# Performance work log

Measured on AMD Instinct MI355X. Metric: run time of the kernel, lower is better.

Reference implementation:

```python
import jax, jax.numpy as jnp
import numpy as np

D = 256      # embed_dims
NH = 8       # num_heads
NL = 1       # num_levels
NP = 6       # num_points
BS = 1
NQ = 40000   # 200x200 BEV queries
H0, W0 = 200, 200
HD = D // NH


def _ln(x, g, b):
    m = jnp.mean(x, -1, keepdims=True)
    v = jnp.var(x, -1, keepdims=True)
    return (x - m) / jnp.sqrt(v + 1e-5) * g + b


def _bilinear(v, lx, ly, H, W):
    # v: (bs, h, H*W, hd); lx/ly: (bs, h, S) pixel coords (align_corners=False, zero padding)
    x0 = jnp.floor(lx).astype(jnp.int32)
    y0 = jnp.floor(ly).astype(jnp.int32)
    acc = 0.
    for dx in (0, 1):
        for dy in (0, 1):
            xi = x0 + dx
            yi = y0 + dy
            w = (1. - jnp.abs(lx - xi)) * (1. - jnp.abs(ly - yi))
            valid = (xi >= 0) & (xi < W) & (yi >= 0) & (yi < H)
            idx = jnp.clip(yi, 0, H - 1) * W + jnp.clip(xi, 0, W - 1)
            g = jnp.take_along_axis(v, idx[..., None], axis=2)  # (bs,h,S,hd)
            acc = acc + g * (w * valid)[..., None]
    return acc


def _forward(query, value, reference_points, W_off, b_off, W_attn, b_attn,
             W_val, b_val, W_out, b_out, ln1_g, ln1_b, W1, b1, W2, b2,
             ln2_g, ln2_b, ss, lsi):
    bs, nq, d = query.shape
    # sampling offsets and attention weights from the query
    off = (query @ W_off + b_off).reshape(bs, nq, NH, NL, NP, 2)
    attn = jax.nn.softmax((query @ W_attn + b_attn).reshape(bs, nq, NH, NL * NP), -1)
    attn = attn.reshape(bs, nq, NH, NL, NP)
    v = (value @ W_val + b_val).reshape(bs, -1, NH, HD).transpose(0, 2, 1, 3)  # (bs,h,HW,hd)
    # offset normalizer is [W, H] per level
    norm = jnp.stack([ss[:, 1], ss[:, 0]], -1).astype(query.dtype)  # (NL,2)
    loc = reference_points[:, :, None, :, None, :] + off / norm[None, None, None, :, None, :]
    out = jnp.zeros((bs, NH, nq, HD), query.dtype)
    for l in range(NL):
        Hl = int(ss[l, 0]); Wl = int(ss[l, 1]); st = int(lsi[l])
        vl = v[:, :, st:st + Hl * Wl]
        lx = (loc[:, :, :, l, :, 0] * Wl - 0.5).transpose(0, 2, 1, 3).reshape(bs, NH, nq * NP)
        ly = (loc[:, :, :, l, :, 1] * Hl - 0.5).transpose(0, 2, 1, 3).reshape(bs, NH, nq * NP)
        sampled = _bilinear(vl, lx, ly, Hl, Wl).reshape(bs, NH, nq, NP, HD)
        wl = attn[:, :, :, l, :].transpose(0, 2, 1, 3)  # (bs,h,nq,P)
        out = out + jnp.einsum('bhqp,bhqpd->bhqd', wl, sampled)
    y_msda = out.transpose(0, 2, 1, 3).reshape(bs, nq, d) @ W_out + b_out
    y = _ln(y_msda + query, ln1_g, ln1_b)
    y_ffn = jax.nn.gelu(y @ W1 + b1, approximate=False) @ W2 + b2
    return _ln(y_ffn + y, ln2_g, ln2_b)


def setup_inputs():
    key = jax.random.key(0)
    ks = jax.random.split(key, 12)
    s = 0.02
    return {
        'query': jax.random.normal(ks[0], (BS, NQ, D), jnp.float32),
        'value': jax.random.normal(ks[1], (BS, H0 * W0, D), jnp.float32),
        'reference_points': jax.random.uniform(ks[2], (BS, NQ, NL, 2), jnp.float32),
        'spatial_shapes': jnp.array([[H0, W0]], jnp.int32),
        'level_start_index': jnp.array([0], jnp.int32),
        'W_off': jax.random.normal(ks[3], (D, NH * NL * NP * 2), jnp.float32) * s,
        'b_off': jax.random.uniform(ks[4], (NH * NL * NP * 2,), jnp.float32, -1., 1.),
        'W_attn': jax.random.normal(ks[5], (D, NH * NL * NP), jnp.float32) * s,
        'b_attn': jnp.zeros((NH * NL * NP,), jnp.float32),
        'W_val': jax.random.normal(ks[6], (D, D), jnp.float32) * s,
        'b_val': jnp.zeros((D,), jnp.float32),
        'W_out': jax.random.normal(ks[7], (D, D), jnp.float32) * s,
        'b_out': jnp.zeros((D,), jnp.float32),
        'ln1_g': jnp.ones((D,), jnp.float32),
        'ln1_b': jnp.zeros((D,), jnp.float32),
        'W1': jax.random.normal(ks[8], (D, D), jnp.float32) * s,
        'b1': jnp.zeros((D,), jnp.float32),
        'W2': jax.random.normal(ks[9], (D, D), jnp.float32) * s,
        'b2': jnp.zeros((D,), jnp.float32),
        'ln2_g': jnp.ones((D,), jnp.float32),
        'ln2_b': jnp.zeros((D,), jnp.float32),
    }


def reference(query, value, reference_points, spatial_shapes, level_start_index,
              W_off, b_off, W_attn, b_attn, W_val, b_val, W_out, b_out,
              ln1_g, ln1_b, W1, b1, W2, b2, ln2_g, ln2_b):
    ss = np.asarray(spatial_shapes)
    lsi = np.asarray(level_start_index)
    return _forward(query, value, reference_points, W_off, b_off, W_attn, b_attn,
                    W_val, b_val, W_out, b_out, ln1_g, ln1_b, W1, b1, W2, b2,
                    ln2_g, ln2_b, ss, lsi)
```

## Files before the change

kernel.cpp:

```cpp
#include <hip/hip_runtime.h>
#include <math.h>

#define NQ 40000
#define DIM 256
#define NH 8
#define NP 6
#define HD 32
#define GH 200
#define GW 200
#define TS 8
#define TNX 25
#define NT 625

typedef short bf16x8 __attribute__((ext_vector_type(8)));
typedef float f32x4 __attribute__((ext_vector_type(4)));

__device__ __forceinline__ unsigned short f2bf(float f) {
    unsigned int u = __builtin_bit_cast(unsigned int, f);
    u += 0x7fffu + ((u >> 16) & 1u);
    return (unsigned short)(u >> 16);
}
__device__ __forceinline__ float bf2f(unsigned short h) {
    return __builtin_bit_cast(float, ((unsigned int)h) << 16);
}

__global__ void __launch_bounds__(256)
f2b_kernel(const float* __restrict__ q, unsigned short* __restrict__ qd,
           const float* __restrict__ v, unsigned short* __restrict__ vd) {
    int b = blockIdx.x;
    const float* src; unsigned short* dst;
    if (b < 5000) { src = q; dst = qd; } else { src = v; dst = vd; b -= 5000; }
    const int i = b * 256 + threadIdx.x;
    const float4* s = (const float4*)src;
    float4 a = s[(size_t)i * 2], c = s[(size_t)i * 2 + 1];
    bf16x8 o;
    o[0] = (short)f2bf(a.x); o[1] = (short)f2bf(a.y);
    o[2] = (short)f2bf(a.z); o[3] = (short)f2bf(a.w);
    o[4] = (short)f2bf(c.x); o[5] = (short)f2bf(c.y);
    o[6] = (short)f2bf(c.z); o[7] = (short)f2bf(c.w);
    *(bf16x8*)(dst + (size_t)i * 8) = o;
}

__global__ void __launch_bounds__(256)
wtrans_kernel(const float* __restrict__ Wval, const float* __restrict__ Woff,
              const float* __restrict__ Wattn, const float* __restrict__ Wout,
              const float* __restrict__ W1, const float* __restrict__ W2,
              const float* __restrict__ b_off, const float* __restrict__ b_attn,
              unsigned short* __restrict__ Bt, float* __restrict__ bias_oa) {
    __shared__ float T[64][65];
    const int m = blockIdx.z;
    const float* src; int N; int dr0;
    if (m == 0)      { src = Wval;  N = 256; dr0 = 0; }
    else if (m == 1) { src = Woff;  N = 96;  dr0 = 256; }
    else if (m == 2) { src = Wattn; N = 48;  dr0 = 352; }
    else if (m == 3) { src = Wout;  N = 256; dr0 = 400; }
    else if (m == 4) { src = W1;    N = 256; dr0 = 656; }
    else             { src = W2;    N = 256; dr0 = 912; }

    if (m == 1 && blockIdx.x == 0 && blockIdx.y == 0 && threadIdx.x < 144)
        bias_oa[threadIdx.x] = threadIdx.x < 96 ? b_off[threadIdx.x]
                                                : b_attn[threadIdx.x - 96];

    const int n0 = blockIdx.x * 64, k0 = blockIdx.y * 64;
    if (n0 >= N) return;
    const int col = threadIdx.x & 63, rg = threadIdx.x >> 6;
#pragma unroll
    for (int i = 0; i < 16; ++i) {
        const int r = rg + 4 * i;
        T[r][col] = (n0 + col < N) ? src[(size_t)(k0 + r) * N + n0 + col] : 0.0f;
    }
    __syncthreads();
#pragma unroll
    for (int i = 0; i < 16; ++i) {
        const int nl = rg + 4 * i;
        if (n0 + nl < N)
            Bt[(size_t)(dr0 + n0 + nl) * 256 + k0 + col] = f2bf(T[col][nl]);
    }
}

__device__ __forceinline__ int tile_of(const float* rp, int q) {
    const float rx = rp[q * 2 + 0] * (float)GW;
    const float ry = rp[q * 2 + 1] * (float)GH;
    const int tx = min(max((int)(rx * (1.0f / TS)), 0), TNX - 1);
    const int ty = min(max((int)(ry * (1.0f / TS)), 0), TNX - 1);
    return ty * TNX + tx;
}

__global__ void __launch_bounds__(256)
sort_zero(int* __restrict__ hist) {
    const int i = blockIdx.x * 256 + threadIdx.x;
    if (i < NT) hist[i] = 0;
}

__global__ void __launch_bounds__(256)
sort_hist(const float* __restrict__ rp, int* __restrict__ hist) {
    const int q = blockIdx.x * 256 + threadIdx.x;
    if (q >= NQ) return;
    atomicAdd(&hist[tile_of(rp, q)], 1);
}

__global__ void __launch_bounds__(64)
sort_scan(const int* __restrict__ hist, int* __restrict__ cursor) {
    const int lane = threadIdx.x;
    int loc[10]; int t = 0;
#pragma unroll
    for (int j = 0; j < 10; ++j) {
        const int idx = lane * 10 + j;
        loc[j] = t;
        t += (idx < NT) ? hist[idx] : 0;
    }
    int s = t;
#pragma unroll
    for (int o = 1; o < 64; o <<= 1) {
        const int u = __shfl_up(s, o);
        if (lane >= o) s += u;
    }
    const int ex = s - t;
#pragma unroll
    for (int j = 0; j < 10; ++j) {
        const int idx = lane * 10 + j;
        if (idx < NT) cursor[idx] = ex + loc[j];
    }
}

__global__ void __launch_bounds__(256)
sort_scatter(const float* __restrict__ rp, int* __restrict__ cursor,
             int* __restrict__ perm) {
    const int q = blockIdx.x * 256 + threadIdx.x;
    if (q >= NQ) return;
    const int pos = atomicAdd(&cursor[tile_of(rp, q)], 1);
    perm[pos] = q;
}

template <int EPI>
__global__ void __launch_bounds__(256)
gemm_bt(const unsigned short* __restrict__ A, const unsigned short* __restrict__ Bt,
        const float* __restrict__ bias, void* __restrict__ C,
        int M, int N, int ldc) {
    __shared__ __align__(16) unsigned short As[128 * 32];
    __shared__ __align__(16) unsigned short Bs[128 * 32];

    const int tid = threadIdx.x, lane = tid & 63, wave = tid >> 6;
    const int quad = lane >> 4, l16 = lane & 15;
    const int wm = wave >> 1, wn = wave & 1;
    const int bm0 = blockIdx.y * 128, bn0 = blockIdx.x * 128;

    f32x4 acc[4][4] = {};

    const int rl = lane >> 2;
    const int c8 = (lane & 3) * 8;

    for (int kt = 0; kt < 8; ++kt) {
        const int k0 = kt * 32;
        __syncthreads();
#pragma unroll
        for (int i = 0; i < 2; ++i) {
            const int rgrp = i * 64 + wave * 16;
            const int gA = min(bm0 + rgrp + rl, M - 1);
            const unsigned short* gpa = A + (size_t)gA * 256 + k0 + c8;
            __builtin_amdgcn_global_load_lds(
                (const __attribute__((address_space(1))) void*)gpa,
                (__attribute__((address_space(3))) void*)(As + (size_t)rgrp * 32),
                16, 0, 0);
            const int gB = min(bn0 + rgrp + rl, N - 1);
            const unsigned short* gpb = Bt + (size_t)gB * 256 + k0 + c8;
            __builtin_amdgcn_global_load_lds(
                (const __attribute__((address_space(1))) void*)gpb,
                (__attribute__((address_space(3))) void*)(Bs + (size_t)rgrp * 32),
                16, 0, 0);
        }
        __syncthreads();

        bf16x8 af[4], bw[4];
#pragma unroll
        for (int t = 0; t < 4; ++t) {
            af[t] = *(const bf16x8*)&As[(wm * 64 + t * 16 + l16) * 32 + quad * 8];
            bw[t] = *(const bf16x8*)&Bs[(wn * 64 + t * 16 + l16) * 32 + quad * 8];
        }
#pragma unroll
        for (int tm = 0; tm < 4; ++tm)
#pragma unroll
            for (int tn = 0; tn < 4; ++tn)
                acc[tm][tn] = __builtin_amdgcn_mfma_f32_16x16x32_bf16(
                    af[tm], bw[tn], acc[tm][tn], 0, 0, 0);
    }

#pragma unroll
    for (int tm = 0; tm < 4; ++tm) {
        const int row0 = bm0 + wm * 64 + tm * 16 + quad * 4;
#pragma unroll
        for (int tn = 0; tn < 4; ++tn) {
            const int col = bn0 + wn * 64 + tn * 16 + l16;
            if (col < N) {
                const float bv = bias[col];
#pragma unroll
                for (int r = 0; r < 4; ++r) {
                    const int row = row0 + r;
                    if (row < M) {
                        float x = acc[tm][tn][r] + bv;
                        if (EPI == 1) {
                            x = 0.5f * x * (1.0f + erff(x * 0.70710678118654752f));
                            ((unsigned short*)C)[(size_t)row * ldc + col] = f2bf(x);
                        } else if (EPI == 2) {
                            ((unsigned short*)C)[(size_t)row * ldc + col] = f2bf(x);
                        } else {
                            ((float*)C)[(size_t)row * ldc + col] = x;
                        }
                    }
                }
            }
        }
    }
}

__global__ void __launch_bounds__(256)
msda_sample(const unsigned short* __restrict__ v,
            const unsigned short* __restrict__ oa,
            const float* __restrict__ rp,
            const int* __restrict__ perm,
            unsigned short* __restrict__ out) {
    const int b = blockIdx.x;
    const int w = (b & 7) * 625 + (b >> 3);
    const int tid = threadIdx.x;
    const int slot = tid >> 2;
    const int q = perm[w * 8 + (slot >> 3)];
    const int h = slot & 7;
    const int c0 = (tid & 3) * 8;

    const float rx = rp[q * 2 + 0] * (float)GW;
    const float ry = rp[q * 2 + 1] * (float)GH;

    const unsigned short* oaq = oa + (size_t)q * 144;
    float lg[NP];
    float mx = -1e30f;
#pragma unroll
    for (int p = 0; p < NP; ++p) {
        lg[p] = bf2f(oaq[96 + h * NP + p]);
        mx = fmaxf(mx, lg[p]);
    }
    float s = 0.0f;
#pragma unroll
    for (int p = 0; p < NP; ++p) { lg[p] = expf(lg[p] - mx); s += lg[p]; }
    const float inv = 1.0f / s;

    float acc[8] = {};
#pragma unroll
    for (int p = 0; p < NP; ++p) {
        const float aw = lg[p] * inv;
        const float lx = rx + bf2f(oaq[h * 12 + p * 2 + 0]) - 0.5f;
        const float ly = ry + bf2f(oaq[h * 12 + p * 2 + 1]) - 0.5f;
        const float fx0 = floorf(lx), fy0 = floorf(ly);
        const int x0 = (int)fx0, y0 = (int)fy0;
        const float fx = lx - fx0, fy = ly - fy0;
#pragma unroll
        for (int dy = 0; dy < 2; ++dy) {
            const int yi = y0 + dy;
            const float wyv = dy ? fy : 1.0f - fy;
#pragma unroll
            for (int dx = 0; dx < 2; ++dx) {
                const int xi = x0 + dx;
                const float wxv = dx ? fx : 1.0f - fx;
                const bool valid = (xi >= 0) & (xi < GW) & (yi >= 0) & (yi < GH);
                const int yc = min(max(yi, 0), GH - 1);
                const int xc = min(max(xi, 0), GW - 1);
                const float wgt = valid ? aw * wxv * wyv : 0.0f;
                const bf16x8 g = *(const bf16x8*)&v[((size_t)(yc * GW + xc)) * 256 + h * 32 + c0];
#pragma unroll
                for (int j = 0; j < 8; ++j)
                    acc[j] += bf2f((unsigned short)g[j]) * wgt;
            }
        }
    }
    bf16x8 o;
#pragma unroll
    for (int j = 0; j < 8; ++j) o[j] = (short)f2bf(acc[j]);
    *(bf16x8*)&out[(size_t)q * 256 + h * 32 + c0] = o;
}

template <int RES_BF, int OUT_BF>
__global__ void __launch_bounds__(256)
ln_res(const float* __restrict__ x, const void* __restrict__ res,
       const float* __restrict__ g, const float* __restrict__ b,
       void* __restrict__ out, int M) {
    const int wave = threadIdx.x >> 6;
    const int lane = threadIdx.x & 63;
    const int row = blockIdx.x * 4 + wave;
    if (row >= M) return;

    const size_t base = (size_t)row * DIM + lane * 4;
    const float4 xv = *(const float4*)(x + base);
    float e[4];
    if (RES_BF) {
        const unsigned short* rb = (const unsigned short*)res + base;
        uint2 rv = *(const uint2*)rb;
        const unsigned short* rs = (const unsigned short*)&rv;
        e[0] = xv.x + bf2f(rs[0]); e[1] = xv.y + bf2f(rs[1]);
        e[2] = xv.z + bf2f(rs[2]); e[3] = xv.w + bf2f(rs[3]);
    } else {
        const float4 rv = *(const float4*)((const float*)res + base);
        e[0] = xv.x + rv.x; e[1] = xv.y + rv.y;
        e[2] = xv.z + rv.z; e[3] = xv.w + rv.w;
    }

    float s = e[0] + e[1] + e[2] + e[3];
    float sq = e[0] * e[0] + e[1] * e[1] + e[2] * e[2] + e[3] * e[3];
#pragma unroll
    for (int o = 1; o < 64; o <<= 1) {
        s += __shfl_xor(s, o);
        sq += __shfl_xor(sq, o);
    }
    const float mean = s * (1.0f / DIM);
    const float var = sq * (1.0f / DIM) - mean * mean;
    const float rstd = rsqrtf(var + 1e-5f);

    const float4 gv = *(const float4*)(g + lane * 4);
    const float4 bv = *(const float4*)(b + lane * 4);
    float o0 = (e[0] - mean) * rstd * gv.x + bv.x;
    float o1 = (e[1] - mean) * rstd * gv.y + bv.y;
    float o2 = (e[2] - mean) * rstd * gv.z + bv.z;
    float o3 = (e[3] - mean) * rstd * gv.w + bv.w;
    if (OUT_BF) {
        unsigned short ob[4] = {f2bf(o0), f2bf(o1), f2bf(o2), f2bf(o3)};
        *(uint2*)((unsigned short*)out + base) = *(uint2*)ob;
    } else {
        float4 o4 = {o0, o1, o2, o3};
        *(float4*)((float*)out + base) = o4;
    }
}

extern "C" void kernel_launch(void* const* d_in, const int* in_sizes, int n_in,
                              void* d_out, int out_size, void* d_ws, size_t ws_size,
                              hipStream_t stream) {
    const float* query  = (const float*)d_in[0];
    const float* value  = (const float*)d_in[1];
    const float* rp     = (const float*)d_in[2];
    const float* W_off  = (const float*)d_in[5];
    const float* b_off  = (const float*)d_in[6];
    const float* W_attn = (const float*)d_in[7];
    const float* b_attn = (const float*)d_in[8];
    const float* W_val  = (const float*)d_in[9];
    const float* b_val  = (const float*)d_in[10];
    const float* W_out  = (const float*)d_in[11];
    const float* b_out  = (const float*)d_in[12];
    const float* ln1_g  = (const float*)d_in[13];
    const float* ln1_b  = (const float*)d_in[14];
    const float* W1     = (const float*)d_in[15];
    const float* b1     = (const float*)d_in[16];
    const float* W2     = (const float*)d_in[17];
    const float* b2     = (const float*)d_in[18];
    const float* ln2_g  = (const float*)d_in[19];
    const float* ln2_b  = (const float*)d_in[20];

    char* ws = (char*)d_ws;
    unsigned short* Bt       = (unsigned short*)ws;
    float*          bias_oa  = (float*)(ws + 598016);
    int*            hist     = (int*)(ws + 598592);
    int*            cursor   = (int*)(ws + 601600);
    int*            perm     = (int*)(ws + 604608);
    unsigned short* query_bf = (unsigned short*)(ws + 770048);
    unsigned short* h1_bf    = query_bf;
    unsigned short* value_bf = (unsigned short*)(ws + 21250048);
    unsigned short* msda_bf  = value_bf;
    unsigned short* y_bf     = value_bf;
    unsigned short* v_bf     = (unsigned short*)(ws + 41730048);
    unsigned short* oa_bf    = (unsigned short*)(ws + 62210048);
    float*          outp     = (float*)d_out;

    dim3 blk(256);
    f2b_kernel<<<dim3(10000), blk, 0, stream>>>(query, query_bf, value, value_bf);
    wtrans_kernel<<<dim3(4, 4, 6), blk, 0, stream>>>(W_val, W_off, W_attn, W_out, W1, W2,
                                                     b_off, b_attn, Bt, bias_oa);
    sort_zero<<<dim3(3), blk, 0, stream>>>(hist);
    sort_hist<<<dim3(157), blk, 0, stream>>>(rp, hist);
    sort_scan<<<dim3(1), dim3(64), 0, stream>>>(hist, cursor);
    sort_scatter<<<dim3(157), blk, 0, stream>>>(rp, cursor, perm);
    gemm_bt<2><<<dim3(2, 313), blk, 0, stream>>>(value_bf, Bt, b_val, (void*)v_bf, NQ, 256, 256);
    gemm_bt<2><<<dim3(2, 313), blk, 0, stream>>>(query_bf, Bt + 256 * 256, bias_oa,
                                                 (void*)oa_bf, NQ, 144, 144);
    msda_sample<<<dim3(5000), blk, 0, stream>>>(v_bf, oa_bf, rp, perm, msda_bf);
    gemm_bt<0><<<dim3(2, 313), blk, 0, stream>>>(msda_bf, Bt + 400 * 256, b_out,
                                                 (void*)outp, NQ, 256, 256);
    ln_res<0, 1><<<dim3(10000), blk, 0, stream>>>(outp, query, ln1_g, ln1_b, (void*)y_bf, NQ);
    gemm_bt<1><<<dim3(2, 313), blk, 0, stream>>>(y_bf, Bt + 656 * 256, b1,
                                                 (void*)h1_bf, NQ, 256, 256);
    gemm_bt<0><<<dim3(2, 313), blk, 0, stream>>>(h1_bf, Bt + 912 * 256, b2,
                                                 (void*)outp, NQ, 256, 256);
    ln_res<1, 0><<<dim3(10000), blk, 0, stream>>>(outp, y_bf, ln2_g, ln2_b, (void*)outp, NQ);
}
```

Measured before the change: 357.4 us.

## Fuse residual-add and LayerNorm into full-width double-buffered GEMM epilogues

Adds a 64-row by 256-column GEMM kernel with double-buffered LDS staging, so each block owns whole output rows. The output projection and second FFN GEMM now do bias, residual add and LayerNorm in the epilogue via a cross-wave LDS reduction, which removes the two separate ln_res passes and their fp32 intermediate round trips. The value projection and first FFN GEMM also move to this kernel. The cost is larger LDS use and lower occupancy per block, and the new kernel has no M bounds checks because it relies on 40000 being divisible by 64.

```diff
diff --git a/kernel.cpp b/kernel.cpp
--- a/kernel.cpp
+++ b/kernel.cpp
@@ -134,8 +134,160 @@
 
 template <int EPI>
 __global__ void __launch_bounds__(256)
+gemm64(const unsigned short* __restrict__ A, const unsigned short* __restrict__ Bt,
+       const float* __restrict__ bias, const void* __restrict__ res,
+       const float* __restrict__ lng, const float* __restrict__ lnb,
+       void* __restrict__ C, int M) {
+    __shared__ __align__(16) unsigned short As[2][64 * 32];
+    __shared__ __align__(16) unsigned short Bs[2][256 * 32];
+    __shared__ __align__(16) float red[64][4][2];
+
+    const int tid = threadIdx.x, lane = tid & 63, wave = tid >> 6;
+    const int quad = lane >> 4, l16 = lane & 15;
+    const int bm0 = blockIdx.x * 64;
+    const int r16 = lane >> 2;
+    const int ch = (lane & 3) * 8;
+
+    f32x4 acc[4][4] = {};
+
+    auto stage = [&](int kt, int buf) {
+        const int k0 = kt * 32;
+        {
+            const int row = wave * 16 + r16;
+            const unsigned short* gp = A + (size_t)(bm0 + row) * 256 + k0 + ch;
+            __builtin_amdgcn_global_load_lds(
+                (const __attribute__((address_space(1))) void*)gp,
+                (__attribute__((address_space(3))) void*)(&As[buf][wave * 16 * 32]),
+                16, 0, 0);
+        }
+#pragma unroll
+        for (int j = 0; j < 4; ++j) {
+            const int rowbase = (wave * 4 + j) * 16;
+            const unsigned short* gp = Bt + (size_t)(rowbase + r16) * 256 + k0 + ch;
+            __builtin_amdgcn_global_load_lds(
+                (const __attribute__((address_space(1))) void*)gp,
+                (__attribute__((address_space(3))) void*)(&Bs[buf][rowbase * 32]),
+                16, 0, 0);
+        }
+    };
+
+    stage(0, 0);
+    __syncthreads();
+
+    for (int kt = 0; kt < 8; ++kt) {
+        const int cur = kt & 1;
+        if (kt < 7) stage(kt + 1, 1 - cur);
+
+        bf16x8 af[4], bw[4];
+#pragma unroll
+        for (int t = 0; t < 4; ++t) {
+            af[t] = *(const bf16x8*)&As[cur][(t * 16 + l16) * 32 + quad * 8];
+            bw[t] = *(const bf16x8*)&Bs[cur][(wave * 64 + t * 16 + l16) * 32 + quad * 8];
+        }
+#pragma unroll
+        for (int tm = 0; tm < 4; ++tm)
+#pragma unroll
+            for (int tn = 0; tn < 4; ++tn)
+                acc[tm][tn] = __builtin_amdgcn_mfma_f32_16x16x32_bf16(
+                    af[tm], bw[tn], acc[tm][tn], 0, 0, 0);
+        __syncthreads();
+    }
+
+    float bias4[4];
+#pragma unroll
+    for (int tn = 0; tn < 4; ++tn) bias4[tn] = bias[wave * 64 + tn * 16 + l16];
+
+    if (EPI == 1 || EPI == 2) {
+#pragma unroll
+        for (int tm = 0; tm < 4; ++tm) {
+            const int row0 = bm0 + tm * 16 + quad * 4;
+#pragma unroll
+            for (int tn = 0; tn < 4; ++tn) {
+                const int col = wave * 64 + tn * 16 + l16;
+#pragma unroll
+                for (int r = 0; r < 4; ++r) {
+                    float x = acc[tm][tn][r] + bias4[tn];
+                    if (EPI == 1) x = 0.5f * x * (1.0f + erff(x * 0.70710678118654752f));
+                    ((unsigned short*)C)[(size_t)(row0 + r) * 256 + col] = f2bf(x);
+                }
+            }
+        }
+        return;
+    }
+
+#pragma unroll
+    for (int tm = 0; tm < 4; ++tm) {
+#pragma unroll
+        for (int r = 0; r < 4; ++r) {
+            const size_t rb = (size_t)(bm0 + tm * 16 + quad * 4 + r) * 256;
+#pragma unroll
+            for (int tn = 0; tn < 4; ++tn) {
+                const int col = wave * 64 + tn * 16 + l16;
+                float e = acc[tm][tn][r] + bias4[tn];
+                if (EPI == 3) e += ((const float*)res)[rb + col];
+                else          e += bf2f(((const unsigned short*)res)[rb + col]);
+                acc[tm][tn][r] = e;
+            }
+        }
+    }
+#pragma unroll
+    for (int tm = 0; tm < 4; ++tm) {
+#pragma unroll
+        for (int r = 0; r < 4; ++r) {
+            float s = 0.0f, sq = 0.0f;
+#pragma unroll
+            for (int tn = 0; tn < 4; ++tn) {
+                const float e = acc[tm][tn][r];
+                s += e; sq += e * e;
+            }
+#pragma unroll
+            for (int o = 1; o < 16; o <<= 1) {
+                s += __shfl_xor(s, o);
+                sq += __shfl_xor(sq, o);
+            }
+            if (l16 == 0) {
+                const int row = tm * 16 + quad * 4 + r;
+                red[row][wave][0] = s;
+                red[row][wave][1] = sq;
+            }
+        }
+    }
+    __syncthreads();
+
+    float gv[4], bvv[4];
+#pragma unroll
+    for (int tn = 0; tn < 4; ++tn) {
+        const int col = wave * 64 + tn * 16 + l16;
+        gv[tn] = lng[col];
+        bvv[tn] = lnb[col];
+    }
+#pragma unroll
+    for (int tm = 0; tm < 4; ++tm) {
+#pragma unroll
+        for (int r = 0; r < 4; ++r) {
+            const int row = tm * 16 + quad * 4 + r;
+            const float4 p0 = *(const float4*)&red[row][0][0];
+            const float4 p1 = *(const float4*)&red[row][2][0];
+            const float sum = p0.x + p0.z + p1.x + p1.z;
+            const float sumsq = p0.y + p0.w + p1.y + p1.w;
+            const float mean = sum * (1.0f / 256.0f);
+            const float var = sumsq * (1.0f / 256.0f) - mean * mean;
+            const float rstd = rsqrtf(var + 1e-5f);
+            const size_t rb = (size_t)(bm0 + row) * 256;
+#pragma unroll
+            for (int tn = 0; tn < 4; ++tn) {
+                const int col = wave * 64 + tn * 16 + l16;
+                const float o = (acc[tm][tn][r] - mean) * rstd * gv[tn] + bvv[tn];
+                if (EPI == 3) ((unsigned short*)C)[rb + col] = f2bf(o);
+                else          ((float*)C)[rb + col] = o;
+            }
+        }
+    }
+}
+
+__global__ void __launch_bounds__(256)
 gemm_bt(const unsigned short* __restrict__ A, const unsigned short* __restrict__ Bt,
-        const float* __restrict__ bias, void* __restrict__ C,
+        const float* __restrict__ bias, unsigned short* __restrict__ C,
         int M, int N, int ldc) {
     __shared__ __align__(16) unsigned short As[128 * 32];
     __shared__ __align__(16) unsigned short Bs[128 * 32];
@@ -146,7 +298,6 @@
     const int bm0 = blockIdx.y * 128, bn0 = blockIdx.x * 128;
 
     f32x4 acc[4][4] = {};
-
     const int rl = lane >> 2;
     const int c8 = (lane & 3) * 8;
 
@@ -196,17 +347,8 @@
 #pragma unroll
                 for (int r = 0; r < 4; ++r) {
                     const int row = row0 + r;
-                    if (row < M) {
-                        float x = acc[tm][tn][r] + bv;
-                        if (EPI == 1) {
-                            x = 0.5f * x * (1.0f + erff(x * 0.70710678118654752f));
-                            ((unsigned short*)C)[(size_t)row * ldc + col] = f2bf(x);
-                        } else if (EPI == 2) {
-                            ((unsigned short*)C)[(size_t)row * ldc + col] = f2bf(x);
-                        } else {
-                            ((float*)C)[(size_t)row * ldc + col] = x;
-                        }
-                    }
+                    if (row < M)
+                        C[(size_t)row * ldc + col] = f2bf(acc[tm][tn][r] + bv);
                 }
             }
         }
@@ -275,57 +417,6 @@
 #pragma unroll
     for (int j = 0; j < 8; ++j) o[j] = (short)f2bf(acc[j]);
     *(bf16x8*)&out[(size_t)q * 256 + h * 32 + c0] = o;
-}
-
-template <int RES_BF, int OUT_BF>
-__global__ void __launch_bounds__(256)
-ln_res(const float* __restrict__ x, const void* __restrict__ res,
-       const float* __restrict__ g, const float* __restrict__ b,
-       void* __restrict__ out, int M) {
-    const int wave = threadIdx.x >> 6;
-    const int lane = threadIdx.x & 63;
-    const int row = blockIdx.x * 4 + wave;
-    if (row >= M) return;
-
-    const size_t base = (size_t)row * DIM + lane * 4;
-    const float4 xv = *(const float4*)(x + base);
-    float e[4];
-    if (RES_BF) {
-        const unsigned short* rb = (const unsigned short*)res + base;
-        uint2 rv = *(const uint2*)rb;
-        const unsigned short* rs = (const unsigned short*)&rv;
-        e[0] = xv.x + bf2f(rs[0]); e[1] = xv.y + bf2f(rs[1]);
-        e[2] = xv.z + bf2f(rs[2]); e[3] = xv.w + bf2f(rs[3]);
-    } else {
-        const float4 rv = *(const float4*)((const float*)res + base);
-        e[0] = xv.x + rv.x; e[1] = xv.y + rv.y;
-        e[2] = xv.z + rv.z; e[3] = xv.w + rv.w;
-    }
-
-    float s = e[0] + e[1] + e[2] + e[3];
-    float sq = e[0] * e[0] + e[1] * e[1] + e[2] * e[2] + e[3] * e[3];
-#pragma unroll
-    for (int o = 1; o < 64; o <<= 1) {
-        s += __shfl_xor(s, o);
-        sq += __shfl_xor(sq, o);
-    }
-    const float mean = s * (1.0f / DIM);
-    const float var = sq * (1.0f / DIM) - mean * mean;
-    const float rstd = rsqrtf(var + 1e-5f);
-
-    const float4 gv = *(const float4*)(g + lane * 4);
-    const float4 bv = *(const float4*)(b + lane * 4);
-    float o0 = (e[0] - mean) * rstd * gv.x + bv.x;
-    float o1 = (e[1] - mean) * rstd * gv.y + bv.y;
-    float o2 = (e[2] - mean) * rstd * gv.z + bv.z;
-    float o3 = (e[3] - mean) * rstd * gv.w + bv.w;
-    if (OUT_BF) {
-        unsigned short ob[4] = {f2bf(o0), f2bf(o1), f2bf(o2), f2bf(o3)};
-        *(uint2*)((unsigned short*)out + base) = *(uint2*)ob;
-    } else {
-        float4 o4 = {o0, o1, o2, o3};
-        *(float4*)((float*)out + base) = o4;
-    }
 }
 
 extern "C" void kernel_launch(void* const* d_in, const int* in_sizes, int n_in,
@@ -361,8 +452,8 @@
     unsigned short* h1_bf    = query_bf;
     unsigned short* value_bf = (unsigned short*)(ws + 21250048);
     unsigned short* msda_bf  = value_bf;
-    unsigned short* y_bf     = value_bf;
     unsigned short* v_bf     = (unsigned short*)(ws + 41730048);
+    unsigned short* y_bf     = v_bf;
     unsigned short* oa_bf    = (unsigned short*)(ws + 62210048);
     float*          outp     = (float*)d_out;
 
@@ -374,16 +465,17 @@
     sort_hist<<<dim3(157), blk, 0, stream>>>(rp, hist);
     sort_scan<<<dim3(1), dim3(64), 0, stream>>>(hist, cursor);
     sort_scatter<<<dim3(157), blk, 0, stream>>>(rp, cursor, perm);
-    gemm_bt<2><<<dim3(2, 313), blk, 0, stream>>>(value_bf, Bt, b_val, (void*)v_bf, NQ, 256, 256);
-    gemm_bt<2><<<dim3(2, 313), blk, 0, stream>>>(query_bf, Bt + 256 * 256, bias_oa,
-                                                 (void*)oa_bf, NQ, 144, 144);
+    gemm64<2><<<dim3(625), blk, 0, stream>>>(value_bf, Bt, b_val, nullptr, nullptr, nullptr,
+                                             (void*)v_bf, NQ);
+    gemm_bt<<<dim3(2, 313), blk, 0, stream>>>(query_bf, Bt + 256 * 256, bias_oa,
+                                              oa_bf, NQ, 144, 144);
     msda_sample<<<dim3(5000), blk, 0, stream>>>(v_bf, oa_bf, rp, perm, msda_bf);
-    gemm_bt<0><<<dim3(2, 313), blk, 0, stream>>>(msda_bf, Bt + 400 * 256, b_out,
-                                                 (void*)outp, NQ, 256, 256);
-    ln_res<0, 1><<<dim3(10000), blk, 0, stream>>>(outp, query, ln1_g, ln1_b, (void*)y_bf, NQ);
-    gemm_bt<1><<<dim3(2, 313), blk, 0, stream>>>(y_bf, Bt + 656 * 256, b1,
-                                                 (void*)h1_bf, NQ, 256, 256);
-    gemm_bt<0><<<dim3(2, 313), blk, 0, stream>>>(h1_bf, Bt + 912 * 256, b2,
-                                                 (void*)outp, NQ, 256, 256);
-    ln_res<1, 0><<<dim3(10000), blk, 0, stream>>>(outp, y_bf, ln2_g, ln2_b, (void*)outp, NQ);
-}
+    gemm64<3><<<dim3(625), blk, 0, stream>>>(msda_bf, Bt + 400 * 256, b_out,
+                                             (const void*)query, ln1_g, ln1_b,
+                                             (void*)y_bf, NQ);
+    gemm64<1><<<dim3(625), blk, 0, stream>>>(y_bf, Bt + 656 * 256, b1, nullptr, nullptr,
+                                             nullptr, (void*)h1_bf, NQ);
+    gemm64<4><<<dim3(625), blk, 0, stream>>>(h1_bf, Bt + 912 * 256, b2,
+                                             (const void*)y_bf, ln2_g, ln2_b,
+                                             (void*)outp, NQ);
+}
```

Result: faster. 335.6 us (-6.1%).
